# Kernel optimization log

Hardware: AMD Instinct MI355X
Metric: run time of the kernel (lower is better)

Reference implementation:

```python
import jax, jax.numpy as jnp
import numpy as np

B, CIN, REL, OUT, SH, H, W = 8, 256, 16, 64, 8, 56, 56
HW = H * W
K = 7          # window size
DIL = 2        # dilation
EPS = 1e-5


def conv1x1(x, w, b=None):
    # x: [B,C,h,w], w: [O,C]
    y = jnp.einsum('oc,bchw->bohw', w, x)
    if b is not None:
        y = y + b[None, :, None, None]
    return y


def bn_eval(x, g, b, m, v):
    scale = g / jnp.sqrt(v + EPS)
    return x * scale[None, :, None, None] + (b - m * scale)[None, :, None, None]


def unfold49(x, pad_reflect, pad_zero):
    # x: [B,C,H,W] -> [B,C,49,H,W]; 7x7 window, dilation 2, stride 1.
    if pad_reflect:
        x = jnp.pad(x, ((0, 0), (0, 0), (pad_reflect, pad_reflect), (pad_reflect, pad_reflect)), mode='reflect')
    if pad_zero:
        x = jnp.pad(x, ((0, 0), (0, 0), (pad_zero, pad_zero), (pad_zero, pad_zero)))
    patches = [x[:, :, DIL * i:DIL * i + H, DIL * j:DIL * j + W]
               for i in range(K) for j in range(K)]
    return jnp.stack(patches, axis=2)


def setup_inputs() -> dict:
    key = jax.random.key(0)
    ks = jax.random.split(key, 12)
    s_in = 1.0 / np.sqrt(CIN)
    inp = {
        'x': jax.random.normal(ks[0], (B, CIN, H, W), jnp.float32),
        'w1': jax.random.normal(ks[1], (REL, CIN), jnp.float32) * s_in,
        'b1': jax.random.normal(ks[2], (REL,), jnp.float32) * 0.01,
        'w2': jax.random.normal(ks[3], (REL, CIN), jnp.float32) * s_in,
        'b2': jax.random.normal(ks[4], (REL,), jnp.float32) * 0.01,
        'w3': jax.random.normal(ks[5], (OUT, CIN), jnp.float32) * s_in,
        'b3': jax.random.normal(ks[6], (OUT,), jnp.float32) * 0.01,
        'bn1_g': jax.random.uniform(ks[7], (REL * (K * K + 1),), jnp.float32, 0.5, 1.5),
        'bn1_b': jax.random.normal(ks[8], (REL * (K * K + 1),), jnp.float32) * 0.01,
        'bn1_m': jnp.zeros((REL * (K * K + 1),), jnp.float32),
        'bn1_v': jnp.ones((REL * (K * K + 1),), jnp.float32),
        'wcw1': jax.random.normal(ks[9], (OUT // SH, REL * (K * K + 1)), jnp.float32) * (1.0 / np.sqrt(REL * 50)),
        'bn2_g': jax.random.uniform(ks[10], (OUT // SH,), jnp.float32, 0.5, 1.5),
        'bn2_b': jnp.zeros((OUT // SH,), jnp.float32),
        'bn2_m': jnp.zeros((OUT // SH,), jnp.float32),
        'bn2_v': jnp.ones((OUT // SH,), jnp.float32),
        'wcw2': jax.random.normal(ks[11], (K * K * OUT // SH, OUT // SH), jnp.float32) * (1.0 / np.sqrt(OUT // SH)),
        'bcw2': jnp.zeros((K * K * OUT // SH,), jnp.float32),
    }
    return inp


def reference(x, w1, b1, w2, b2, w3, b3, bn1_g, bn1_b, bn1_m, bn1_v,
              wcw1, bn2_g, bn2_b, bn2_m, bn2_v, wcw2, bcw2):
    x1 = conv1x1(x, w1, b1)                      # [B,REL,H,W]
    x2 = conv1x1(x, w2, b2)                      # [B,REL,H,W]
    x3 = conv1x1(x, w3, b3)                      # [B,OUT,H,W]

    # x1 -> [B,REL,1,HW]
    x1f = x1.reshape(B, REL, 1, HW)
    # x2: ReflectionPad2d(2) then Unfold(7, dilation=2, padding=4) -> [B,REL*49,1,HW]
    x2u = unfold49(x2, pad_reflect=2, pad_zero=4).reshape(B, REL * K * K, 1, HW)

    cat = jnp.concatenate([x1f, x2u], axis=1)    # [B, REL*50, 1, HW]
    t = jax.nn.relu(bn_eval(cat, bn1_g, bn1_b, bn1_m, bn1_v))
    t = conv1x1(t, wcw1)                         # [B, OUT/SH, 1, HW], no bias
    t = jax.nn.relu(bn_eval(t, bn2_g, bn2_b, bn2_m, bn2_v))
    wmap = conv1x1(t, wcw2, bcw2)                # [B, 49*OUT/SH, 1, HW]
    wmap = wmap.reshape(B, OUT // SH, K * K, HW)  # channel layout wc*49+k

    # Aggregation(7, 1, 6, 2, pad_mode=1): reflect-pad 6, 7x7 dilated unfold,
    # out[b,c,n] = sum_k unf[b,c,k,n] * w[b, c//SH, k, n]
    x3u = unfold49(x3, pad_reflect=6, pad_zero=0).reshape(B, OUT // SH, SH, K * K, HW)
    out = jnp.einsum('bgskn,bgkn->bgsn', x3u, wmap).reshape(B, OUT, H, W)
    return out
```

## Files before the change

### kernel.cpp

```cpp
#include <hip/hip_runtime.h>
#include <hip/hip_bf16.h>

#define HW    3136
#define HH    56
#define NCIN  256
#define KK    49
#define PH    68
#define PP    (PH*PH)

#define OFF_WT    0
#define OFF_BCAT  24576
#define OFF_TAB   24672
#define OFF_WTAB  34272
#define OFF_B2F   38976
#define OFF_X1    39040
#define OFF_X2P   440448
#define OFF_X3P   1032320

__global__ __launch_bounds__(256) void kprep(
    const float* __restrict__ w1, const float* __restrict__ b1,
    const float* __restrict__ w2, const float* __restrict__ b2,
    const float* __restrict__ w3, const float* __restrict__ b3,
    const float* __restrict__ bn1g, const float* __restrict__ bn1b,
    const float* __restrict__ bn1m, const float* __restrict__ bn1v,
    const float* __restrict__ wcw1,
    const float* __restrict__ bn2g, const float* __restrict__ bn2b,
    const float* __restrict__ bn2m, const float* __restrict__ bn2v,
    const float* __restrict__ wcw2, const float* __restrict__ bcw2,
    float* __restrict__ ws)
{
    int idx = blockIdx.x * 256 + threadIdx.x;
    if (idx < 24576) {
        int o = idx >> 8, c = idx & 255;
        float v = (o < 16) ? w1[o * 256 + c]
                : (o < 32) ? w2[(o - 16) * 256 + c]
                           : w3[(o - 32) * 256 + c];
        ws[OFF_WT + c * 96 + o] = v;
    }
    int i2 = idx - 24576;
    if (i2 >= 0 && i2 < 96) {
        float v = (i2 < 16) ? b1[i2] : (i2 < 32) ? b2[i2 - 16] : b3[i2 - 32];
        ws[OFF_BCAT + i2] = v;
    }
    int i3 = idx - 24672;
    if (i3 >= 0 && i3 < 9600) {
        int row = i3 / 12, c = i3 - row * 12;
        int uu = row >> 4, r = row & 15;
        int j = (uu < 49) ? (16 + r * KK + uu) : r;
        float val = 0.f;
        if (c == 0) {
            val = bn1g[j] / sqrtf(bn1v[j] + 1e-5f);
        } else if (c == 1) {
            float s = bn1g[j] / sqrtf(bn1v[j] + 1e-5f);
            val = bn1b[j] - bn1m[j] * s;
        } else if (c < 10) {
            int e = c - 2;
            float s2 = bn2g[e] / sqrtf(bn2v[e] + 1e-5f);
            val = wcw1[e * 800 + j] * s2;
        }
        ws[OFF_TAB + i3] = val;
    }
    int i4 = idx - 34272;
    if (i4 >= 0 && i4 < 4704) {
        int row = i4 / 12, c = i4 - row * 12;
        float val = 0.f;
        if (c == 0)      val = bcw2[row];
        else if (c < 9)  val = wcw2[row * 8 + (c - 1)];
        ws[OFF_WTAB + i4] = val;
    }
    int i5 = idx - 38976;
    if (i5 >= 0 && i5 < 8) {
        float s2 = bn2g[i5] / sqrtf(bn2v[i5] + 1e-5f);
        ws[OFF_B2F + i5] = bn2b[i5] - bn2m[i5] * s2;
    }
}

__global__ __launch_bounds__(512) void kconv(
    const float* __restrict__ x, const float* __restrict__ wT,
    const float* __restrict__ bcat, float* __restrict__ x1out,
    float* __restrict__ x2pad, float* __restrict__ x3pad)
{
    __shared__ float xl[64][64];
    const int tid = threadIdx.x;
    const int l   = tid & 63;
    const int wv  = __builtin_amdgcn_readfirstlane(tid >> 6);
    const int b   = blockIdx.x / 49;
    const int hw0 = (blockIdx.x % 49) * 64;
    const int ob  = wv * 12;

    {
        int z = (blockIdx.x % 49) * 336 + tid;
        if (tid < 336 && z < 16384) {
            int ch = z >> 10, cell = z & 1023;
            int p, q;
            if (cell < 272)      { p = cell / 68;          q = cell - p * 68; }
            else if (cell < 544) { int cc = cell - 272; p = 64 + cc / 68; q = cc - (p - 64) * 68; }
            else                 { int cc = cell - 544; p = 4 + (cc >> 3); int qq = cc & 7; q = (qq < 4) ? qq : 60 + qq; }
            x2pad[((size_t)b * 16 + ch) * PP + p * PH + q] = 0.f;
        }
    }

    float acc[12];
    const float* bc = bcat + ob;
#pragma unroll
    for (int i = 0; i < 12; ++i) acc[i] = bc[i];

    const float* xb = x + (size_t)b * NCIN * HW + hw0;

    for (int cc = 0; cc < 4; ++cc) {
        __syncthreads();
#pragma unroll
        for (int i = 0; i < 8; ++i)
            xl[i * 8 + wv][l] = xb[(size_t)(cc * 64 + i * 8 + wv) * HW + l];
        __syncthreads();

        const float* wp = wT + (cc * 64) * 96 + ob;
#pragma unroll 4
        for (int k = 0; k < 64; ++k) {
            float xv = xl[k][l];
            const float4* wq = (const float4*)(wp + k * 96);
            float4 A = wq[0], B = wq[1], C = wq[2];
            acc[0]  = fmaf(xv, A.x, acc[0]);  acc[1]  = fmaf(xv, A.y, acc[1]);
            acc[2]  = fmaf(xv, A.z, acc[2]);  acc[3]  = fmaf(xv, A.w, acc[3]);
            acc[4]  = fmaf(xv, B.x, acc[4]);  acc[5]  = fmaf(xv, B.y, acc[5]);
            acc[6]  = fmaf(xv, B.z, acc[6]);  acc[7]  = fmaf(xv, B.w, acc[7]);
            acc[8]  = fmaf(xv, C.x, acc[8]);  acc[9]  = fmaf(xv, C.y, acc[9]);
            acc[10] = fmaf(xv, C.z, acc[10]); acc[11] = fmaf(xv, C.w, acc[11]);
        }
    }

    const int n  = hw0 + l;
    const int y  = n / HH;
    const int xx = n - y * HH;
    const int p0 = y + 6, q0 = xx + 6;
    const int yr3 = (y >= 1 && y <= 6) ? 6 - y : ((y >= 49 && y <= 54) ? 116 - y : -1);
    const int xr3 = (xx >= 1 && xx <= 6) ? 6 - xx : ((xx >= 49 && xx <= 54) ? 116 - xx : -1);
    const int yr2 = (y == 1 || y == 2) ? 6 - y : ((y == 53 || y == 54) ? 116 - y : -1);
    const int xr2 = (xx == 1 || xx == 2) ? 6 - xx : ((xx == 53 || xx == 54) ? 116 - xx : -1);

#pragma unroll
    for (int i = 0; i < 12; ++i) {
        const int ch = ob + i;
        const float v = acc[i];
        if (ch < 16) {
            x1out[((size_t)b * 16 + ch) * HW + n] = v;
        } else if (ch < 32) {
            float* pl = x2pad + ((size_t)b * 16 + (ch - 16)) * PP;
            pl[p0 * PH + q0] = v;
            if (yr2 >= 0)              pl[yr2 * PH + q0]  = v;
            if (xr2 >= 0)              pl[p0 * PH + xr2]  = v;
            if (yr2 >= 0 && xr2 >= 0)  pl[yr2 * PH + xr2] = v;
        } else {
            float* pl = x3pad + ((size_t)b * 64 + (ch - 32)) * PP;
            pl[p0 * PH + q0] = v;
            if (yr3 >= 0)              pl[yr3 * PH + q0]  = v;
            if (xr3 >= 0)              pl[p0 * PH + xr3]  = v;
            if (yr3 >= 0 && xr3 >= 0)  pl[yr3 * PH + xr3] = v;
        }
    }
}

__global__ __launch_bounds__(512) void kmainB(
    const float* __restrict__ x1, const float* __restrict__ x2pad,
    const float* __restrict__ x3pad, const float* __restrict__ tab,
    const float* __restrict__ b2f, const float* __restrict__ wtab,
    float* __restrict__ out)
{
    __shared__ float red[8][8][64];
    __shared__ float tl[8][64];
    const int tid = threadIdx.x;
    const int w   = __builtin_amdgcn_readfirstlane(tid >> 6);
    const int l   = tid & 63;
    const int b   = blockIdx.x / 49;
    const int nb  = (blockIdx.x % 49) * 64;
    const int n   = nb + l;
    const int y   = n / HH;
    const int xx  = n - y * HH;
    const int pbase = y * PH + xx;

    const float* x1b = x1 + (size_t)b * 16 * HW + n;
    const float* x2b = x2pad + (size_t)b * 16 * PP + pbase;

    float acc[8];
#pragma unroll
    for (int g = 0; g < 8; ++g) acc[g] = 0.f;

    const int u0 = (50 * w) >> 3;
    const int u1 = (50 * (w + 1)) >> 3;

#pragma unroll 1
    for (int u = u0; u < u1; ++u) {
        const float* trow;
        const float* xp;
        size_t xstr;
        if (u == 0) {
            trow = tab + 49 * 192;
            xp   = x1b;
            xstr = HW;
        } else {
            const int kk = u - 1;
            const int i  = kk / 7;
            const int jj = kk - i * 7;
            trow = tab + kk * 192;
            xp   = x2b + i * (2 * PH) + jj * 2;
            xstr = PP;
        }
#pragma unroll
        for (int r = 0; r < 16; ++r) {
            const float4* tq = (const float4*)(trow + r * 12);
            float4 A = tq[0], Bv = tq[1], Cv = tq[2];
            float v = xp[(size_t)r * xstr];
            v = fmaxf(fmaf(v, A.x, A.y), 0.f);
            acc[0] = fmaf(v, A.z, acc[0]);  acc[1] = fmaf(v, A.w, acc[1]);
            acc[2] = fmaf(v, Bv.x, acc[2]); acc[3] = fmaf(v, Bv.y, acc[3]);
            acc[4] = fmaf(v, Bv.z, acc[4]); acc[5] = fmaf(v, Bv.w, acc[5]);
            acc[6] = fmaf(v, Cv.x, acc[6]); acc[7] = fmaf(v, Cv.y, acc[7]);
        }
    }

#pragma unroll
    for (int g = 0; g < 8; ++g) red[w][g][l] = acc[g];
    __syncthreads();

    {
        const int g  = tid >> 6;
        const int px = tid & 63;
        float s = b2f[g];
#pragma unroll
        for (int ww = 0; ww < 8; ++ww) s += red[ww][g][px];
        tl[g][px] = fmaxf(s, 0.f);
    }
    __syncthreads();

    const int g   = w;
    const int sh  = l >> 5;
    const int pp2 = l & 31;
    const int n0  = nb + pp2 * 2;
    const int y0  = n0 / HH;
    const int xx0 = n0 - y0 * HH;
    const int pb2 = y0 * PH + xx0;

    float t0[8], t1[8];
#pragma unroll
    for (int e = 0; e < 8; ++e) {
        t0[e] = tl[e][pp2 * 2];
        t1[e] = tl[e][pp2 * 2 + 1];
    }

    float2 acc2[4];
#pragma unroll
    for (int s = 0; s < 4; ++s) acc2[s] = make_float2(0.f, 0.f);

    const float* x3b = x3pad + ((size_t)b * 64 + g * 8 + sh * 4) * PP + pb2;
    const float* wg  = wtab + (size_t)g * KK * 12;

#pragma unroll 1
    for (int i = 0; i < 7; ++i) {
        const float* xrow = x3b + i * (2 * PH);
#pragma unroll
        for (int jj = 0; jj < 7; ++jj) {
            const int k = i * 7 + jj;
            const float* wrow = wg + k * 12;
            const float4* wq = (const float4*)wrow;
            float4 A = wq[0], Bv = wq[1];
            float w7 = wrow[8];
            float w0 = A.x, w1 = A.x;
            w0 = fmaf(t0[0], A.y, w0);  w1 = fmaf(t1[0], A.y, w1);
            w0 = fmaf(t0[1], A.z, w0);  w1 = fmaf(t1[1], A.z, w1);
            w0 = fmaf(t0[2], A.w, w0);  w1 = fmaf(t1[2], A.w, w1);
            w0 = fmaf(t0[3], Bv.x, w0); w1 = fmaf(t1[3], Bv.x, w1);
            w0 = fmaf(t0[4], Bv.y, w0); w1 = fmaf(t1[4], Bv.y, w1);
            w0 = fmaf(t0[5], Bv.z, w0); w1 = fmaf(t1[5], Bv.z, w1);
            w0 = fmaf(t0[6], Bv.w, w0); w1 = fmaf(t1[6], Bv.w, w1);
            w0 = fmaf(t0[7], w7, w0);   w1 = fmaf(t1[7], w7, w1);
#pragma unroll
            for (int s = 0; s < 4; ++s) {
                float2 xv = *(const float2*)(xrow + (size_t)s * PP + jj * 2);
                acc2[s].x = fmaf(xv.x, w0, acc2[s].x);
                acc2[s].y = fmaf(xv.y, w1, acc2[s].y);
            }
        }
    }

    float* op = out + ((size_t)b * 64 + g * 8 + sh * 4) * HW + n0;
#pragma unroll
    for (int s = 0; s < 4; ++s)
        *(float2*)(op + (size_t)s * HW) = acc2[s];
}

extern "C" void kernel_launch(void* const* d_in, const int* in_sizes, int n_in,
                              void* d_out, int out_size, void* d_ws, size_t ws_size,
                              hipStream_t stream) {
    const float* x    = (const float*)d_in[0];
    const float* w1   = (const float*)d_in[1];
    const float* b1   = (const float*)d_in[2];
    const float* w2   = (const float*)d_in[3];
    const float* b2   = (const float*)d_in[4];
    const float* w3   = (const float*)d_in[5];
    const float* b3   = (const float*)d_in[6];
    const float* bn1g = (const float*)d_in[7];
    const float* bn1b = (const float*)d_in[8];
    const float* bn1m = (const float*)d_in[9];
    const float* bn1v = (const float*)d_in[10];
    const float* wcw1 = (const float*)d_in[11];
    const float* bn2g = (const float*)d_in[12];
    const float* bn2b = (const float*)d_in[13];
    const float* bn2m = (const float*)d_in[14];
    const float* bn2v = (const float*)d_in[15];
    const float* wcw2 = (const float*)d_in[16];
    const float* bcw2 = (const float*)d_in[17];

    float* ws = (float*)d_ws;

    kprep<<<153, 256, 0, stream>>>(w1, b1, w2, b2, w3, b3,
                                   bn1g, bn1b, bn1m, bn1v, wcw1,
                                   bn2g, bn2b, bn2m, bn2v, wcw2, bcw2, ws);
    kconv<<<392, 512, 0, stream>>>(x, ws + OFF_WT, ws + OFF_BCAT,
                                   ws + OFF_X1, ws + OFF_X2P, ws + OFF_X3P);
    kmainB<<<392, 512, 0, stream>>>(ws + OFF_X1, ws + OFF_X2P, ws + OFF_X3P,
                                    ws + OFF_TAB, ws + OFF_B2F, ws + OFF_WTAB,
                                    (float*)d_out);
}
```

Before: 71.29 us.

## Switch intermediate buffers to channel-last layout with vectorized loads and stores

Result: slower. 98.84 us (+38.6%).

```diff
diff --git a/kernel.cpp b/kernel.cpp
--- a/kernel.cpp
+++ b/kernel.cpp
@@ -85,19 +85,19 @@
     const int l   = tid & 63;
     const int wv  = __builtin_amdgcn_readfirstlane(tid >> 6);
     const int b   = blockIdx.x / 49;
-    const int hw0 = (blockIdx.x % 49) * 64;
+    const int bi  = blockIdx.x % 49;
+    const int hw0 = bi * 64;
     const int ob  = wv * 12;
 
-    {
-        int z = (blockIdx.x % 49) * 336 + tid;
-        if (tid < 336 && z < 16384) {
-            int ch = z >> 10, cell = z & 1023;
-            int p, q;
-            if (cell < 272)      { p = cell / 68;          q = cell - p * 68; }
-            else if (cell < 544) { int cc = cell - 272; p = 64 + cc / 68; q = cc - (p - 64) * 68; }
-            else                 { int cc = cell - 544; p = 4 + (cc >> 3); int qq = cc & 7; q = (qq < 4) ? qq : 60 + qq; }
-            x2pad[((size_t)b * 16 + ch) * PP + p * PH + q] = 0.f;
-        }
+    if (bi < 8) {
+        int z = bi * 512 + tid;
+        int cell = z >> 2, sub = z & 3;
+        int p, q;
+        if (cell < 272)      { p = cell / 68;  q = cell - p * 68; }
+        else if (cell < 544) { int c2 = cell - 272; p = 64 + c2 / 68; q = c2 - (c2 / 68) * 68; }
+        else                 { int c2 = cell - 544; p = 4 + (c2 >> 3); int qq = c2 & 7; q = (qq < 4) ? qq : 60 + qq; }
+        *(float4*)(x2pad + ((size_t)b * PP + p * PH + q) * 16 + sub * 4) =
+            make_float4(0.f, 0.f, 0.f, 0.f);
     }
 
     float acc[12];
@@ -137,25 +137,27 @@
     const int xr3 = (xx >= 1 && xx <= 6) ? 6 - xx : ((xx >= 49 && xx <= 54) ? 116 - xx : -1);
     const int yr2 = (y == 1 || y == 2) ? 6 - y : ((y == 53 || y == 54) ? 116 - y : -1);
     const int xr2 = (xx == 1 || xx == 2) ? 6 - xx : ((xx == 53 || xx == 54) ? 116 - xx : -1);
-
-#pragma unroll
-    for (int i = 0; i < 12; ++i) {
-        const int ch = ob + i;
-        const float v = acc[i];
-        if (ch < 16) {
-            x1out[((size_t)b * 16 + ch) * HW + n] = v;
-        } else if (ch < 32) {
-            float* pl = x2pad + ((size_t)b * 16 + (ch - 16)) * PP;
-            pl[p0 * PH + q0] = v;
-            if (yr2 >= 0)              pl[yr2 * PH + q0]  = v;
-            if (xr2 >= 0)              pl[p0 * PH + xr2]  = v;
-            if (yr2 >= 0 && xr2 >= 0)  pl[yr2 * PH + xr2] = v;
+    const int cell0 = p0 * PH + q0;
+
+#pragma unroll
+    for (int qg = 0; qg < 3; ++qg) {
+        const int ch0 = ob + qg * 4;
+        float4 v = make_float4(acc[qg * 4], acc[qg * 4 + 1],
+                               acc[qg * 4 + 2], acc[qg * 4 + 3]);
+        if (ch0 < 16) {
+            *(float4*)(x1out + ((size_t)b * HW + n) * 16 + ch0) = v;
+        } else if (ch0 < 32) {
+            float* base = x2pad + ((size_t)b * PP) * 16 + (ch0 - 16);
+            *(float4*)(base + (size_t)cell0 * 16) = v;
+            if (yr2 >= 0)             *(float4*)(base + (size_t)(yr2 * PH + q0) * 16)  = v;
+            if (xr2 >= 0)             *(float4*)(base + (size_t)(p0 * PH + xr2) * 16)  = v;
+            if (yr2 >= 0 && xr2 >= 0) *(float4*)(base + (size_t)(yr2 * PH + xr2) * 16) = v;
         } else {
-            float* pl = x3pad + ((size_t)b * 64 + (ch - 32)) * PP;
-            pl[p0 * PH + q0] = v;
-            if (yr3 >= 0)              pl[yr3 * PH + q0]  = v;
-            if (xr3 >= 0)              pl[p0 * PH + xr3]  = v;
-            if (yr3 >= 0 && xr3 >= 0)  pl[yr3 * PH + xr3] = v;
+            float* base = x3pad + ((size_t)b * PP) * 64 + (ch0 - 32);
+            *(float4*)(base + (size_t)cell0 * 64) = v;
+            if (yr3 >= 0)             *(float4*)(base + (size_t)(yr3 * PH + q0) * 64)  = v;
+            if (xr3 >= 0)             *(float4*)(base + (size_t)(p0 * PH + xr3) * 64)  = v;
+            if (yr3 >= 0 && xr3 >= 0) *(float4*)(base + (size_t)(yr3 * PH + xr3) * 64) = v;
         }
     }
 }
@@ -176,10 +178,6 @@
     const int n   = nb + l;
     const int y   = n / HH;
     const int xx  = n - y * HH;
-    const int pbase = y * PH + xx;
-
-    const float* x1b = x1 + (size_t)b * 16 * HW + n;
-    const float* x2b = x2pad + (size_t)b * 16 * PP + pbase;
 
     float acc[8];
 #pragma unroll
@@ -192,25 +190,26 @@
     for (int u = u0; u < u1; ++u) {
         const float* trow;
         const float* xp;
-        size_t xstr;
         if (u == 0) {
             trow = tab + 49 * 192;
-            xp   = x1b;
-            xstr = HW;
+            xp   = x1 + ((size_t)b * HW + n) * 16;
         } else {
             const int kk = u - 1;
             const int i  = kk / 7;
             const int jj = kk - i * 7;
             trow = tab + kk * 192;
-            xp   = x2b + i * (2 * PH) + jj * 2;
-            xstr = PP;
-        }
+            xp   = x2pad + ((size_t)b * PP + (y + 2 * i) * PH + (xx + 2 * jj)) * 16;
+        }
+        float vr[16];
+        *(float4*)&vr[0]  = *(const float4*)xp;
+        *(float4*)&vr[4]  = *(const float4*)(xp + 4);
+        *(float4*)&vr[8]  = *(const float4*)(xp + 8);
+        *(float4*)&vr[12] = *(const float4*)(xp + 12);
 #pragma unroll
         for (int r = 0; r < 16; ++r) {
             const float4* tq = (const float4*)(trow + r * 12);
             float4 A = tq[0], Bv = tq[1], Cv = tq[2];
-            float v = xp[(size_t)r * xstr];
-            v = fmaxf(fmaf(v, A.x, A.y), 0.f);
+            float v = fmaxf(fmaf(vr[r], A.x, A.y), 0.f);
             acc[0] = fmaf(v, A.z, acc[0]);  acc[1] = fmaf(v, A.w, acc[1]);
             acc[2] = fmaf(v, Bv.x, acc[2]); acc[3] = fmaf(v, Bv.y, acc[3]);
             acc[4] = fmaf(v, Bv.z, acc[4]); acc[5] = fmaf(v, Bv.w, acc[5]);
@@ -232,31 +231,21 @@
     }
     __syncthreads();
 
-    const int g   = w;
-    const int sh  = l >> 5;
-    const int pp2 = l & 31;
-    const int n0  = nb + pp2 * 2;
-    const int y0  = n0 / HH;
-    const int xx0 = n0 - y0 * HH;
-    const int pb2 = y0 * PH + xx0;
-
-    float t0[8], t1[8];
-#pragma unroll
-    for (int e = 0; e < 8; ++e) {
-        t0[e] = tl[e][pp2 * 2];
-        t1[e] = tl[e][pp2 * 2 + 1];
-    }
-
-    float2 acc2[4];
-#pragma unroll
-    for (int s = 0; s < 4; ++s) acc2[s] = make_float2(0.f, 0.f);
-
-    const float* x3b = x3pad + ((size_t)b * 64 + g * 8 + sh * 4) * PP + pb2;
+    const int g = w;
+    float t[8];
+#pragma unroll
+    for (int e = 0; e < 8; ++e) t[e] = tl[e][l];
+
+    float a2[8];
+#pragma unroll
+    for (int s = 0; s < 8; ++s) a2[s] = 0.f;
+
+    const float* x3b = x3pad + ((size_t)b * PP) * 64 + (size_t)g * 8;
     const float* wg  = wtab + (size_t)g * KK * 12;
 
 #pragma unroll 1
     for (int i = 0; i < 7; ++i) {
-        const float* xrow = x3b + i * (2 * PH);
+        const int rowc = (y + 2 * i) * PH + xx;
 #pragma unroll
         for (int jj = 0; jj < 7; ++jj) {
             const int k = i * 7 + jj;
@@ -264,28 +253,25 @@
             const float4* wq = (const float4*)wrow;
             float4 A = wq[0], Bv = wq[1];
             float w7 = wrow[8];
-            float w0 = A.x, w1 = A.x;
-            w0 = fmaf(t0[0], A.y, w0);  w1 = fmaf(t1[0], A.y, w1);
-            w0 = fmaf(t0[1], A.z, w0);  w1 = fmaf(t1[1], A.z, w1);
-            w0 = fmaf(t0[2], A.w, w0);  w1 = fmaf(t1[2], A.w, w1);
-            w0 = fmaf(t0[3], Bv.x, w0); w1 = fmaf(t1[3], Bv.x, w1);
-            w0 = fmaf(t0[4], Bv.y, w0); w1 = fmaf(t1[4], Bv.y, w1);
-            w0 = fmaf(t0[5], Bv.z, w0); w1 = fmaf(t1[5], Bv.z, w1);
-            w0 = fmaf(t0[6], Bv.w, w0); w1 = fmaf(t1[6], Bv.w, w1);
-            w0 = fmaf(t0[7], w7, w0);   w1 = fmaf(t1[7], w7, w1);
-#pragma unroll
-            for (int s = 0; s < 4; ++s) {
-                float2 xv = *(const float2*)(xrow + (size_t)s * PP + jj * 2);
-                acc2[s].x = fmaf(xv.x, w0, acc2[s].x);
-                acc2[s].y = fmaf(xv.y, w1, acc2[s].y);
-            }
-        }
-    }
-
-    float* op = out + ((size_t)b * 64 + g * 8 + sh * 4) * HW + n0;
-#pragma unroll
-    for (int s = 0; s < 4; ++s)
-        *(float2*)(op + (size_t)s * HW) = acc2[s];
+            float wv = A.x;
+            wv = fmaf(t[0], A.y, wv);  wv = fmaf(t[1], A.z, wv);
+            wv = fmaf(t[2], A.w, wv);  wv = fmaf(t[3], Bv.x, wv);
+            wv = fmaf(t[4], Bv.y, wv); wv = fmaf(t[5], Bv.z, wv);
+            wv = fmaf(t[6], Bv.w, wv); wv = fmaf(t[7], w7, wv);
+
+            const float* xp = x3b + (size_t)(rowc + 2 * jj) * 64;
+            float4 s0 = *(const float4*)xp;
+            float4 s1 = *(const float4*)(xp + 4);
+            a2[0] = fmaf(s0.x, wv, a2[0]); a2[1] = fmaf(s0.y, wv, a2[1]);
+            a2[2] = fmaf(s0.z, wv, a2[2]); a2[3] = fmaf(s0.w, wv, a2[3]);
+            a2[4] = fmaf(s1.x, wv, a2[4]); a2[5] = fmaf(s1.y, wv, a2[5]);
+            a2[6] = fmaf(s1.z, wv, a2[6]); a2[7] = fmaf(s1.w, wv, a2[7]);
+        }
+    }
+
+    float* op = out + ((size_t)b * 64 + g * 8) * HW + n;
+#pragma unroll
+    for (int s = 0; s < 8; ++s) op[(size_t)s * HW] = a2[s];
 }
 
 extern "C" void kernel_launch(void* const* d_in, const int* in_sizes, int n_in,
```
